# Performance work log

Measured on AMD Instinct MI355X. Metric: run time of the kernel, lower is better.

Reference implementation:

```python
import jax, jax.numpy as jnp
import numpy as np

T, B, E, H = 2048, 4, 1024, 16
HD = E // H
SCALE = HD ** -0.5


def setup_inputs() -> dict:
    key = jax.random.key(0)
    k1, k2, k3 = jax.random.split(key, 3)
    # xavier-ish scaling on weights for numerical sanity
    inputs = jax.random.normal(k1, (T, B, E), dtype=jnp.float32)
    in_proj_weight = jax.random.normal(k2, (3 * E, E), dtype=jnp.float32) * (2.0 / (4 * E)) ** 0.5
    out_proj_weight = jax.random.normal(k3, (E, E), dtype=jnp.float32) * (1.0 / E) ** 0.5
    return {"inputs": inputs, "in_proj_weight": in_proj_weight, "out_proj_weight": out_proj_weight}


def reference(inputs, in_proj_weight, out_proj_weight):
    t, b, e = inputs.shape
    # fused QKV projection: [T,B,E] @ [E,3E] -> [T, B*H, 3, HD]
    qkv = jnp.einsum('tbe,fe->tbf', inputs, in_proj_weight)
    qkv = qkv.reshape(t, b * H, 3, HD)
    q, k, v = qkv[:, :, 0, :], qkv[:, :, 1, :], qkv[:, :, 2, :]  # [T, B*H, HD]
    # scaled attention scores per (batch*head): [B*H, T, T]
    scores = SCALE * jnp.einsum('tnd,snd->nts', q, k)
    probs = jax.nn.softmax(scores, axis=-1)
    # dropout p=0.0 -> identity
    ctx = jnp.einsum('nts,snd->tnd', probs, v).reshape(t, b, e)
    # output projection (applied to attention context, matching intended math / backward)
    return jnp.einsum('tbe,oe->tbo', ctx, out_proj_weight)
```

## Files before the change

kernel.cpp:

```cpp
#include <hip/hip_runtime.h>
#include <stdint.h>
#include <stddef.h>


typedef __attribute__((ext_vector_type(8))) short bf16x8;
typedef __attribute__((ext_vector_type(4))) float f32x4;
typedef __attribute__((ext_vector_type(4))) unsigned int u32x4;

#define MFMA16(a, b, c) __builtin_amdgcn_mfma_f32_16x16x32_bf16((a), (b), (c), 0, 0, 0)

__device__ __forceinline__ unsigned short f2bf(float f) {
  unsigned u = __builtin_bit_cast(unsigned, f);
  u += 0x7fffu + ((u >> 16) & 1u);
  return (unsigned short)(u >> 16);
}

__device__ __forceinline__ float fast_exp2(float x) {
#if __has_builtin(__builtin_amdgcn_exp2f)
  return __builtin_amdgcn_exp2f(x);
#else
  return exp2f(x);
#endif
}

__device__ __forceinline__ unsigned cvtpk(float lo, float hi) {
  unsigned r;
  asm volatile("v_cvt_pk_bf16_f32 %0, %1, %2" : "=v"(r) : "v"(lo), "v"(hi));
  return r;
}

__device__ __forceinline__ void lane_swap32(unsigned &a, unsigned &b) {
#if __has_builtin(__builtin_amdgcn_permlane32_swap)
  auto r = __builtin_amdgcn_permlane32_swap(a, b, false, false);
  a = r[0]; b = r[1];
#else
  const bool hi = (threadIdx.x & 32) != 0;
  unsigned sa = (unsigned)__shfl_xor((int)a, 32, 64);
  unsigned sb = (unsigned)__shfl_xor((int)b, 32, 64);
  unsigned na = hi ? sb : a;
  unsigned nb = hi ? b : sa;
  a = na; b = nb;
#endif
}

__device__ __forceinline__ void lane_swap16(unsigned &a, unsigned &b) {
#if __has_builtin(__builtin_amdgcn_permlane16_swap)
  auto r = __builtin_amdgcn_permlane16_swap(a, b, false, false);
  a = r[0]; b = r[1];
#else
  const bool odd = (threadIdx.x & 16) != 0;
  unsigned sa = (unsigned)__shfl_xor((int)a, 16, 64);
  unsigned sb = (unsigned)__shfl_xor((int)b, 16, 64);
  unsigned na = odd ? sb : a;
  unsigned nb = odd ? b : sa;
  a = na; b = nb;
#endif
}

__device__ __forceinline__ void gload_lds16(const void* g, void* l) {
  __builtin_amdgcn_global_load_lds((const __attribute__((address_space(1))) void*)g,
                                   (__attribute__((address_space(3))) void*)l,
                                   16, 0, 0);
}

__global__ __launch_bounds__(256) void k_cvt3(const float* __restrict__ X,
                                              const float* __restrict__ W1,
                                              const float* __restrict__ Wo,
                                              unsigned short* __restrict__ Xb,
                                              unsigned short* __restrict__ W1b,
                                              unsigned short* __restrict__ Wob) {
  int i = blockIdx.x * 256 + threadIdx.x;
  const float* src;
  unsigned short* dst;
  int j;
  if (i < 2097152) { src = X; dst = Xb; j = i; }
  else if (i < 2097152 + 786432) { src = W1; dst = W1b; j = i - 2097152; }
  else { src = Wo; dst = Wob; j = i - (2097152 + 786432); }
  const float4 v = ((const float4*)src)[j];
  ushort4 o;
  o.x = f2bf(v.x); o.y = f2bf(v.y); o.z = f2bf(v.z); o.w = f2bf(v.w);
  ((ushort4*)dst)[j] = o;
}

__global__ __launch_bounds__(256, 2) void k_gemm_qkv(
    const unsigned short* __restrict__ A,
    const unsigned short* __restrict__ Bt,
    unsigned short* __restrict__ Qb,
    unsigned short* __restrict__ Kb,
    unsigned short* __restrict__ VTb) {
  constexpr int K = 1024;
  __shared__ __align__(16) unsigned short Sm[8704];
  unsigned short* As = Sm;
  unsigned short* Bs = Sm + 4096;

  const int tid = threadIdx.x;
  const int l = tid & 63, w = tid >> 6;
  const int lr = l & 15, lg = l >> 4;
  const int bm = blockIdx.x, bn = blockIdx.y;
  const int wr = (w >> 1) * 64, wc = (w & 1) * 64;

  f32x4 acc[4][4] = {};

  const int o0 = tid * 16, o1 = tid * 16 + 4096;
  const int r0 = o0 >> 6, c0 = o0 & 63;
  const int r1 = o1 >> 6, c1 = o1 & 63;
  const char* gA0 = (const char*)A + (size_t)(bm * 128 + r0) * (K * 2) + c0;
  const char* gA1 = (const char*)A + (size_t)(bm * 128 + r1) * (K * 2) + c1;
  const char* gB0 = (const char*)Bt + (size_t)(bn * 128 + r0) * (K * 2) + c0;
  const char* gB1 = (const char*)Bt + (size_t)(bn * 128 + r1) * (K * 2) + c1;
  char* lA0 = (char*)As + o0;
  char* lA1 = (char*)As + o1;
  char* lB0 = (char*)Bs + o0;
  char* lB1 = (char*)Bs + o1;

  for (int kt = 0; kt < K / 32; ++kt) {
    const int kb = kt * 64;
    gload_lds16(gA0 + kb, lA0);
    gload_lds16(gA1 + kb, lA1);
    gload_lds16(gB0 + kb, lB0);
    gload_lds16(gB1 + kb, lB1);
    __syncthreads();
    bf16x8 af[4], bfr[4];
#pragma unroll
    for (int mf = 0; mf < 4; ++mf)
      af[mf] = *(const bf16x8*)&As[(wr + mf * 16 + lr) * 32 + lg * 8];
#pragma unroll
    for (int nf = 0; nf < 4; ++nf)
      bfr[nf] = *(const bf16x8*)&Bs[(wc + nf * 16 + lr) * 32 + lg * 8];
#pragma unroll
    for (int mf = 0; mf < 4; ++mf)
#pragma unroll
      for (int nf = 0; nf < 4; ++nf)
        acc[mf][nf] = MFMA16(af[mf], bfr[nf], acc[mf][nf]);
    __syncthreads();
  }

  const int f0 = bn * 128 + wc;
  const int s3g = (f0 >> 6) % 3;
  const int hqg = f0 / 192;

  if (s3g != 2) {
    unsigned short* dst = (s3g == 0) ? Qb : Kb;
    const float qscale = (s3g == 0) ? 0.18033688011112042f : 1.0f;
#pragma unroll
    for (int nf = 0; nf < 4; ++nf) {
      const int d = nf * 16 + lr;
#pragma unroll
      for (int mf = 0; mf < 4; ++mf) {
#pragma unroll
        for (int i = 0; i < 4; ++i) {
          const int r = bm * 128 + wr + mf * 16 + lg * 4 + i;
          const int t = r >> 2, bb2 = r & 3;
          dst[((size_t)(bb2 * 16 + hqg) * 2048 + t) * 64 + d] = f2bf(acc[mf][nf][i] * qscale);
        }
      }
    }
  } else {
#pragma unroll
    for (int nf = 0; nf < 4; ++nf) {
      const int d = nf * 16 + lr;
#pragma unroll
      for (int mf = 0; mf < 4; ++mf) {
#pragma unroll
        for (int i = 0; i < 4; ++i) {
          const int rl = wr + mf * 16 + lg * 4 + i;
          Sm[rl * 68 + d] = f2bf(acc[mf][nf][i]);
        }
      }
    }
  }
  __syncthreads();
  if (s3g == 2) {
    const int u = (w >> 1) * 64 + l;
    const int d = u >> 1, th = u & 1;
#pragma unroll
    for (int bb = 0; bb < 4; ++bb) {
      const size_t base = ((size_t)(bb * 16 + hqg) * 64 + d) * 2048 + bm * 32 + th * 16;
#pragma unroll
      for (int tq = 0; tq < 4; ++tq) {
        ushort4 pk;
        pk.x = Sm[((th * 16 + tq * 4 + 0) * 4 + bb) * 68 + d];
        pk.y = Sm[((th * 16 + tq * 4 + 1) * 4 + bb) * 68 + d];
        pk.z = Sm[((th * 16 + tq * 4 + 2) * 4 + bb) * 68 + d];
        pk.w = Sm[((th * 16 + tq * 4 + 3) * 4 + bb) * 68 + d];
        *(ushort4*)&VTb[base + tq * 4] = pk;
      }
    }
  }
}

__global__ __launch_bounds__(256, 2) void k_attn(
    const unsigned short* __restrict__ Qb, const unsigned short* __restrict__ Kb,
    const unsigned short* __restrict__ VTb, unsigned short* __restrict__ Cx) {
  __shared__ __align__(16) unsigned short Ks[2][64 * 64];
  __shared__ __align__(16) unsigned short Vt[2][64 * 64];

  const int tid = threadIdx.x;
  const int l = tid & 63, w = tid >> 6;
  const int lq = l & 15, lg = l >> 4;
  const int n = blockIdx.x, qt = blockIdx.y;

  const unsigned short* Qh = Qb + (size_t)n * (2048 * 64);
  const unsigned short* Kh = Kb + (size_t)n * (2048 * 64);
  const unsigned short* Vh = VTb + (size_t)n * (64 * 2048);

  bf16x8 aq[4][2];
#pragma unroll
  for (int qf = 0; qf < 4; ++qf)
#pragma unroll
    for (int kd = 0; kd < 2; ++kd)
      aq[qf][kd] = *(const bf16x8*)&Qh[(size_t)(qt * 256 + w * 64 + qf * 16 + lq) * 64 +
                                       kd * 32 + lg * 8];

  f32x4 o[4][4] = {};
  float lsum[4] = {0.f, 0.f, 0.f, 0.f};

  char* Ksl = (char*)&Ks[0][0];
  char* Vtl = (char*)&Vt[0][0];

  auto STAGE = [&](int buf, int st) {
    const int s0 = st * 64;
#pragma unroll
    for (int it = 0; it < 2; ++it) {
      const int off = (it * 256 + tid) * 16;
      const int row = off >> 7;
      const int colb = (off & 127) ^ ((row & 7) << 4);
      gload_lds16((const char*)Kh + ((size_t)(s0 + row) << 7) + colb, Ksl + buf * 8192 + off);
      gload_lds16((const char*)Vh + ((size_t)row << 12) + (s0 << 1) + colb, Vtl + buf * 8192 + off);
    }
  };

  STAGE(0, 0);
  asm volatile("s_waitcnt vmcnt(0)" ::: "memory");
  __builtin_amdgcn_s_barrier();

#pragma unroll 2
  for (int st = 0; st < 32; ++st) {
    const int cur = st & 1;
    if (st + 1 < 32) STAGE(cur ^ 1, st + 1);

    const char* Kc = Ksl + cur * 8192;
    const char* Vc = Vtl + cur * 8192;

    __builtin_amdgcn_s_setprio(1);
#pragma unroll
    for (int kb = 0; kb < 2; ++kb) {
      bf16x8 kf[2][2];
#pragma unroll
      for (int sfl = 0; sfl < 2; ++sfl) {
        const int rowk = (2 * kb + sfl) * 16 + lq;
        const int sw = (rowk & 7) << 4;
        kf[sfl][0] = *(const bf16x8*)(Kc + ((rowk * 128 + lg * 16) ^ sw));
        kf[sfl][1] = *(const bf16x8*)(Kc + ((rowk * 128 + 64 + lg * 16) ^ sw));
      }

      bf16x8 pq[4];
#pragma unroll
      for (int qf = 0; qf < 4; ++qf) {
        f32x4 s0 = {0.f, 0.f, 0.f, 0.f};
        f32x4 s1 = {0.f, 0.f, 0.f, 0.f};
        s0 = MFMA16(kf[0][0], aq[qf][0], s0);
        s0 = MFMA16(kf[0][1], aq[qf][1], s0);
        s1 = MFMA16(kf[1][0], aq[qf][0], s1);
        s1 = MFMA16(kf[1][1], aq[qf][1], s1);
        float accs = 0.f;
#pragma unroll
        for (int i = 0; i < 4; ++i) {
          s0[i] = fast_exp2(s0[i]);
          s1[i] = fast_exp2(s1[i]);
          accs += s0[i] + s1[i];
        }
        lsum[qf] += accs;
        unsigned w0 = cvtpk(s0[0], s0[1]);
        unsigned w1 = cvtpk(s0[2], s0[3]);
        unsigned w2 = cvtpk(s1[0], s1[1]);
        unsigned w3 = cvtpk(s1[2], s1[3]);
        lane_swap32(w0, w2);
        lane_swap32(w1, w3);
        lane_swap16(w0, w2);
        lane_swap16(w1, w3);
        u32x4 t4 = {w0, w1, w2, w3};
        pq[qf] = __builtin_bit_cast(bf16x8, t4);
      }

#pragma unroll
      for (int df = 0; df < 4; ++df) {
        const int rowd = df * 16 + lq;
        const int sw = (rowd & 7) << 4;
        bf16x8 vf = *(const bf16x8*)(Vc + ((rowd * 128 + kb * 64 + lg * 16) ^ sw));
#pragma unroll
        for (int qf = 0; qf < 4; ++qf)
          o[df][qf] = MFMA16(vf, pq[qf], o[df][qf]);
      }
    }
    __builtin_amdgcn_s_setprio(0);

    asm volatile("s_waitcnt vmcnt(0)" ::: "memory");
    __builtin_amdgcn_s_barrier();
  }

  const int bb = n >> 4, h = n & 15;
#pragma unroll
  for (int qf = 0; qf < 4; ++qf) {
    float li = lsum[qf];
    li += __shfl_xor(li, 16, 64);
    li += __shfl_xor(li, 32, 64);
    const float inv = 1.0f / li;
    const int q = qt * 256 + w * 64 + qf * 16 + lq;
#pragma unroll
    for (int df = 0; df < 4; ++df) {
      ushort4 pk;
      pk.x = f2bf(o[df][qf][0] * inv);
      pk.y = f2bf(o[df][qf][1] * inv);
      pk.z = f2bf(o[df][qf][2] * inv);
      pk.w = f2bf(o[df][qf][3] * inv);
      *(ushort4*)&Cx[(size_t)(q * 4 + bb) * 1024 + h * 64 + df * 16 + lg * 4] = pk;
    }
  }
}

__global__ __launch_bounds__(256, 2) void k_gemm_out(
    const unsigned short* __restrict__ A,
    const unsigned short* __restrict__ Bt,
    float* __restrict__ C) {
  constexpr int K = 1024;
  __shared__ __align__(16) unsigned short As[128 * 32];
  __shared__ __align__(16) unsigned short Bs[128 * 32];
  const int tid = threadIdx.x;
  const int l = tid & 63, w = tid >> 6;
  const int lr = l & 15, lg = l >> 4;
  const int bm = blockIdx.x, bn = blockIdx.y;
  const int wr = (w >> 1) * 64, wc = (w & 1) * 64;

  f32x4 acc[4][4] = {};

  const int o0 = tid * 16, o1 = tid * 16 + 4096;
  const int r0 = o0 >> 6, c0 = o0 & 63;
  const int r1 = o1 >> 6, c1 = o1 & 63;
  const char* gA0 = (const char*)A + (size_t)(bm * 128 + r0) * (K * 2) + c0;
  const char* gA1 = (const char*)A + (size_t)(bm * 128 + r1) * (K * 2) + c1;
  const char* gB0 = (const char*)Bt + (size_t)(bn * 128 + r0) * (K * 2) + c0;
  const char* gB1 = (const char*)Bt + (size_t)(bn * 128 + r1) * (K * 2) + c1;
  char* lA0 = (char*)As + o0;
  char* lA1 = (char*)As + o1;
  char* lB0 = (char*)Bs + o0;
  char* lB1 = (char*)Bs + o1;

  for (int kt = 0; kt < K / 32; ++kt) {
    const int kb = kt * 64;
    gload_lds16(gA0 + kb, lA0);
    gload_lds16(gA1 + kb, lA1);
    gload_lds16(gB0 + kb, lB0);
    gload_lds16(gB1 + kb, lB1);
    __syncthreads();
    bf16x8 af[4], bfr[4];
#pragma unroll
    for (int mf = 0; mf < 4; ++mf)
      af[mf] = *(const bf16x8*)&As[(wr + mf * 16 + lr) * 32 + lg * 8];
#pragma unroll
    for (int nf = 0; nf < 4; ++nf)
      bfr[nf] = *(const bf16x8*)&Bs[(wc + nf * 16 + lr) * 32 + lg * 8];
#pragma unroll
    for (int mf = 0; mf < 4; ++mf)
#pragma unroll
      for (int nf = 0; nf < 4; ++nf)
        acc[mf][nf] = MFMA16(af[mf], bfr[nf], acc[mf][nf]);
    __syncthreads();
  }

#pragma unroll
  for (int mf = 0; mf < 4; ++mf)
#pragma unroll
    for (int i = 0; i < 4; ++i) {
      const int r = bm * 128 + wr + mf * 16 + lg * 4 + i;
#pragma unroll
      for (int nf = 0; nf < 4; ++nf)
        C[(size_t)r * 1024 + bn * 128 + wc + nf * 16 + lr] = acc[mf][nf][i];
    }
}

extern "C" void kernel_launch(void* const* d_in, const int* in_sizes, int n_in,
                              void* d_out, int out_size, void* d_ws, size_t ws_size,
                              hipStream_t stream) {
  const float* X = (const float*)d_in[0];
  const float* W1 = (const float*)d_in[1];
  const float* Wo = (const float*)d_in[2];
  float* out = (float*)d_out;

  char* ws = (char*)d_ws;
  unsigned short* Xb  = (unsigned short*)(ws);
  unsigned short* W1b = (unsigned short*)(ws + 16777216);
  unsigned short* Wob = (unsigned short*)(ws + 23068672);
  unsigned short* Qb  = (unsigned short*)(ws + 25165824);
  unsigned short* Kb  = (unsigned short*)(ws + 41943040);
  unsigned short* VTb = (unsigned short*)(ws + 58720256);
  unsigned short* Cx  = (unsigned short*)(ws + 75497472);

  k_cvt3<<<12288, 256, 0, stream>>>(X, W1, Wo, Xb, W1b, Wob);
  k_gemm_qkv<<<dim3(64, 24), 256, 0, stream>>>(Xb, W1b, Qb, Kb, VTb);
  k_attn<<<dim3(64, 8), 256, 0, stream>>>(Qb, Kb, VTb, Cx);
  k_gemm_out<<<dim3(64, 8), 256, 0, stream>>>(Cx, Wob, out);
}
```

Before: 186.7 us.

## Rewrite projection GEMMs with 128x256 tiles, double-buffered swizzled LDS and prefetch

Both the QKV and output projection GEMMs now use 512-thread blocks computing 128x256 tiles over a K step of 64. Global-to-LDS loads for the next step are issued while the current step runs its MFMAs, using a double buffer, vmcnt waits, raw barriers and setprio. The LDS layout is XOR-swizzled to avoid bank conflicts. This cuts barrier count and exposed load latency per FLOP, but uses 96KB of LDS per block, which may limit occupancy, and halves the number of blocks.

```diff
diff --git a/kernel.cpp b/kernel.cpp
--- a/kernel.cpp
+++ b/kernel.cpp
@@ -82,60 +82,85 @@
   ((ushort4*)dst)[j] = o;
 }
 
-__global__ __launch_bounds__(256, 2) void k_gemm_qkv(
+
+__global__ __launch_bounds__(512, 2) void k_gemm_qkv(
     const unsigned short* __restrict__ A,
     const unsigned short* __restrict__ Bt,
     unsigned short* __restrict__ Qb,
     unsigned short* __restrict__ Kb,
     unsigned short* __restrict__ VTb) {
-  constexpr int K = 1024;
-  __shared__ __align__(16) unsigned short Sm[8704];
-  unsigned short* As = Sm;
-  unsigned short* Bs = Sm + 4096;
+  __shared__ __align__(16) char Sm[98304];
+  char* lAs = Sm;
+  char* lBs = Sm + 32768;
 
   const int tid = threadIdx.x;
-  const int l = tid & 63, w = tid >> 6;
+  const int l = tid & 63;
+  const int wid = tid >> 6;
   const int lr = l & 15, lg = l >> 4;
+  const int wr = wid >> 2, wc = wid & 3;
   const int bm = blockIdx.x, bn = blockIdx.y;
-  const int wr = (w >> 1) * 64, wc = (w & 1) * 64;
 
   f32x4 acc[4][4] = {};
-
-  const int o0 = tid * 16, o1 = tid * 16 + 4096;
-  const int r0 = o0 >> 6, c0 = o0 & 63;
-  const int r1 = o1 >> 6, c1 = o1 & 63;
-  const char* gA0 = (const char*)A + (size_t)(bm * 128 + r0) * (K * 2) + c0;
-  const char* gA1 = (const char*)A + (size_t)(bm * 128 + r1) * (K * 2) + c1;
-  const char* gB0 = (const char*)Bt + (size_t)(bn * 128 + r0) * (K * 2) + c0;
-  const char* gB1 = (const char*)Bt + (size_t)(bn * 128 + r1) * (K * 2) + c1;
-  char* lA0 = (char*)As + o0;
-  char* lA1 = (char*)As + o1;
-  char* lB0 = (char*)Bs + o0;
-  char* lB1 = (char*)Bs + o1;
-
-  for (int kt = 0; kt < K / 32; ++kt) {
-    const int kb = kt * 64;
-    gload_lds16(gA0 + kb, lA0);
-    gload_lds16(gA1 + kb, lA1);
-    gload_lds16(gB0 + kb, lB0);
-    gload_lds16(gB1 + kb, lB1);
-    __syncthreads();
-    bf16x8 af[4], bfr[4];
-#pragma unroll
-    for (int mf = 0; mf < 4; ++mf)
-      af[mf] = *(const bf16x8*)&As[(wr + mf * 16 + lr) * 32 + lg * 8];
-#pragma unroll
-    for (int nf = 0; nf < 4; ++nf)
-      bfr[nf] = *(const bf16x8*)&Bs[(wc + nf * 16 + lr) * 32 + lg * 8];
-#pragma unroll
-    for (int mf = 0; mf < 4; ++mf)
+  const int colF = (lg * 16) ^ (((lr >> 1) & 3) << 4);
+
+  auto STAGE_A = [&](int buf, int kt2, int uk) {
+    const int row = tid >> 2;
+    const int colb = (tid & 3) * 16;
+    const int sw = ((row >> 1) & 3) << 4;
+    gload_lds16((const char*)A + (size_t)(bm * 128 + row) * 2048 + kt2 * 128 + uk * 64 +
+                    (colb ^ sw),
+                lAs + (buf * 2 + uk) * 8192 + tid * 16);
+  };
+  auto STAGE_B = [&](int buf, int kt2, int uk) {
+#pragma unroll
+    for (int i = 0; i < 2; ++i) {
+      const int idx = i * 512 + tid;
+      const int row = idx >> 2;
+      const int colb = (idx & 3) * 16;
+      const int sw = ((row >> 1) & 3) << 4;
+      gload_lds16((const char*)Bt + (size_t)(bn * 256 + row) * 2048 + kt2 * 128 + uk * 64 +
+                      (colb ^ sw),
+                  lBs + (buf * 2 + uk) * 16384 + idx * 16);
+    }
+  };
+
+  STAGE_A(0, 0, 0); STAGE_B(0, 0, 0);
+  STAGE_A(0, 0, 1); STAGE_B(0, 0, 1);
+  asm volatile("s_waitcnt vmcnt(3)" ::: "memory");
+  __builtin_amdgcn_s_barrier();
+
+#pragma unroll 2
+  for (int kt = 0; kt < 16; ++kt) {
+    const int buf = kt & 1, nbuf = buf ^ 1;
+    const int ktn = (kt + 1 < 16) ? kt + 1 : 15;
+
+#pragma unroll
+    for (int uk = 0; uk < 2; ++uk) {
+      bf16x8 a[4], b[4];
+#pragma unroll
+      for (int mf = 0; mf < 4; ++mf)
+        a[mf] = *(const bf16x8*)(lAs + (buf * 2 + uk) * 8192 + (wr * 64 + mf * 16 + lr) * 64 + colF);
 #pragma unroll
       for (int nf = 0; nf < 4; ++nf)
-        acc[mf][nf] = MFMA16(af[mf], bfr[nf], acc[mf][nf]);
-    __syncthreads();
-  }
-
-  const int f0 = bn * 128 + wc;
+        b[nf] = *(const bf16x8*)(lBs + (buf * 2 + uk) * 16384 + (wc * 64 + nf * 16 + lr) * 64 + colF);
+      STAGE_A(nbuf, ktn, uk);
+      STAGE_B(nbuf, ktn, uk);
+      __builtin_amdgcn_s_setprio(1);
+#pragma unroll
+      for (int mf = 0; mf < 4; ++mf)
+#pragma unroll
+        for (int nf = 0; nf < 4; ++nf)
+          acc[mf][nf] = MFMA16(a[mf], b[nf], acc[mf][nf]);
+      __builtin_amdgcn_s_setprio(0);
+      asm volatile("s_waitcnt vmcnt(3)" ::: "memory");
+      __builtin_amdgcn_s_barrier();
+    }
+  }
+
+  asm volatile("s_waitcnt vmcnt(0)" ::: "memory");
+  __syncthreads();
+
+  const int f0 = bn * 256 + wc * 64;
   const int s3g = (f0 >> 6) % 3;
   const int hqg = f0 / 192;
 
@@ -149,13 +174,14 @@
       for (int mf = 0; mf < 4; ++mf) {
 #pragma unroll
         for (int i = 0; i < 4; ++i) {
-          const int r = bm * 128 + wr + mf * 16 + lg * 4 + i;
+          const int r = bm * 128 + wr * 64 + mf * 16 + lg * 4 + i;
           const int t = r >> 2, bb2 = r & 3;
           dst[((size_t)(bb2 * 16 + hqg) * 2048 + t) * 64 + d] = f2bf(acc[mf][nf][i] * qscale);
         }
       }
     }
   } else {
+    unsigned short* Tb = (unsigned short*)(Sm + wc * 24576);
 #pragma unroll
     for (int nf = 0; nf < 4; ++nf) {
       const int d = nf * 16 + lr;
@@ -163,15 +189,16 @@
       for (int mf = 0; mf < 4; ++mf) {
 #pragma unroll
         for (int i = 0; i < 4; ++i) {
-          const int rl = wr + mf * 16 + lg * 4 + i;
-          Sm[rl * 68 + d] = f2bf(acc[mf][nf][i]);
+          const int rl = wr * 64 + mf * 16 + lg * 4 + i;
+          Tb[rl * 68 + d] = f2bf(acc[mf][nf][i]);
         }
       }
     }
   }
   __syncthreads();
   if (s3g == 2) {
-    const int u = (w >> 1) * 64 + l;
+    unsigned short* Tb = (unsigned short*)(Sm + wc * 24576);
+    const int u = wr * 64 + l;
     const int d = u >> 1, th = u & 1;
 #pragma unroll
     for (int bb = 0; bb < 4; ++bb) {
@@ -179,14 +206,99 @@
 #pragma unroll
       for (int tq = 0; tq < 4; ++tq) {
         ushort4 pk;
-        pk.x = Sm[((th * 16 + tq * 4 + 0) * 4 + bb) * 68 + d];
-        pk.y = Sm[((th * 16 + tq * 4 + 1) * 4 + bb) * 68 + d];
-        pk.z = Sm[((th * 16 + tq * 4 + 2) * 4 + bb) * 68 + d];
-        pk.w = Sm[((th * 16 + tq * 4 + 3) * 4 + bb) * 68 + d];
+        pk.x = Tb[((th * 16 + tq * 4 + 0) * 4 + bb) * 68 + d];
+        pk.y = Tb[((th * 16 + tq * 4 + 1) * 4 + bb) * 68 + d];
+        pk.z = Tb[((th * 16 + tq * 4 + 2) * 4 + bb) * 68 + d];
+        pk.w = Tb[((th * 16 + tq * 4 + 3) * 4 + bb) * 68 + d];
         *(ushort4*)&VTb[base + tq * 4] = pk;
       }
     }
   }
+}
+
+__global__ __launch_bounds__(512, 2) void k_gemm_out(
+    const unsigned short* __restrict__ A,
+    const unsigned short* __restrict__ Bt,
+    float* __restrict__ C) {
+  __shared__ __align__(16) char Sm[98304];
+  char* lAs = Sm;
+  char* lBs = Sm + 32768;
+
+  const int tid = threadIdx.x;
+  const int l = tid & 63;
+  const int wid = tid >> 6;
+  const int lr = l & 15, lg = l >> 4;
+  const int wr = wid >> 2, wc = wid & 3;
+  const int bm = blockIdx.x, bn = blockIdx.y;
+
+  f32x4 acc[4][4] = {};
+  const int colF = (lg * 16) ^ (((lr >> 1) & 3) << 4);
+
+  auto STAGE_A = [&](int buf, int kt2, int uk) {
+    const int row = tid >> 2;
+    const int colb = (tid & 3) * 16;
+    const int sw = ((row >> 1) & 3) << 4;
+    gload_lds16((const char*)A + (size_t)(bm * 128 + row) * 2048 + kt2 * 128 + uk * 64 +
+                    (colb ^ sw),
+                lAs + (buf * 2 + uk) * 8192 + tid * 16);
+  };
+  auto STAGE_B = [&](int buf, int kt2, int uk) {
+#pragma unroll
+    for (int i = 0; i < 2; ++i) {
+      const int idx = i * 512 + tid;
+      const int row = idx >> 2;
+      const int colb = (idx & 3) * 16;
+      const int sw = ((row >> 1) & 3) << 4;
+      gload_lds16((const char*)Bt + (size_t)(bn * 256 + row) * 2048 + kt2 * 128 + uk * 64 +
+                      (colb ^ sw),
+                  lBs + (buf * 2 + uk) * 16384 + idx * 16);
+    }
+  };
+
+  STAGE_A(0, 0, 0); STAGE_B(0, 0, 0);
+  STAGE_A(0, 0, 1); STAGE_B(0, 0, 1);
+  asm volatile("s_waitcnt vmcnt(3)" ::: "memory");
+  __builtin_amdgcn_s_barrier();
+
+#pragma unroll 2
+  for (int kt = 0; kt < 16; ++kt) {
+    const int buf = kt & 1, nbuf = buf ^ 1;
+    const int ktn = (kt + 1 < 16) ? kt + 1 : 15;
+
+#pragma unroll
+    for (int uk = 0; uk < 2; ++uk) {
+      bf16x8 a[4], b[4];
+#pragma unroll
+      for (int mf = 0; mf < 4; ++mf)
+        a[mf] = *(const bf16x8*)(lAs + (buf * 2 + uk) * 8192 + (wr * 64 + mf * 16 + lr) * 64 + colF);
+#pragma unroll
+      for (int nf = 0; nf < 4; ++nf)
+        b[nf] = *(const bf16x8*)(lBs + (buf * 2 + uk) * 16384 + (wc * 64 + nf * 16 + lr) * 64 + colF);
+      STAGE_A(nbuf, ktn, uk);
+      STAGE_B(nbuf, ktn, uk);
+      __builtin_amdgcn_s_setprio(1);
+#pragma unroll
+      for (int mf = 0; mf < 4; ++mf)
+#pragma unroll
+        for (int nf = 0; nf < 4; ++nf)
+          acc[mf][nf] = MFMA16(a[mf], b[nf], acc[mf][nf]);
+      __builtin_amdgcn_s_setprio(0);
+      asm volatile("s_waitcnt vmcnt(3)" ::: "memory");
+      __builtin_amdgcn_s_barrier();
+    }
+  }
+
+  asm volatile("s_waitcnt vmcnt(0)" ::: "memory");
+
+#pragma unroll
+  for (int mf = 0; mf < 4; ++mf)
+#pragma unroll
+    for (int i = 0; i < 4; ++i) {
+      const int r = bm * 128 + wr * 64 + mf * 16 + lg * 4 + i;
+#pragma unroll
+      for (int nf = 0; nf < 4; ++nf)
+        C[(size_t)r * 1024 + bn * 256 + wc * 64 + nf * 16 + lr] = acc[mf][nf][i];
+    }
 }
 
 __global__ __launch_bounds__(256, 2) void k_attn(
@@ -319,66 +431,6 @@
   }
 }
 
-__global__ __launch_bounds__(256, 2) void k_gemm_out(
-    const unsigned short* __restrict__ A,
-    const unsigned short* __restrict__ Bt,
-    float* __restrict__ C) {
-  constexpr int K = 1024;
-  __shared__ __align__(16) unsigned short As[128 * 32];
-  __shared__ __align__(16) unsigned short Bs[128 * 32];
-  const int tid = threadIdx.x;
-  const int l = tid & 63, w = tid >> 6;
-  const int lr = l & 15, lg = l >> 4;
-  const int bm = blockIdx.x, bn = blockIdx.y;
-  const int wr = (w >> 1) * 64, wc = (w & 1) * 64;
-
-  f32x4 acc[4][4] = {};
-
-  const int o0 = tid * 16, o1 = tid * 16 + 4096;
-  const int r0 = o0 >> 6, c0 = o0 & 63;
-  const int r1 = o1 >> 6, c1 = o1 & 63;
-  const char* gA0 = (const char*)A + (size_t)(bm * 128 + r0) * (K * 2) + c0;
-  const char* gA1 = (const char*)A + (size_t)(bm * 128 + r1) * (K * 2) + c1;
-  const char* gB0 = (const char*)Bt + (size_t)(bn * 128 + r0) * (K * 2) + c0;
-  const char* gB1 = (const char*)Bt + (size_t)(bn * 128 + r1) * (K * 2) + c1;
-  char* lA0 = (char*)As + o0;
-  char* lA1 = (char*)As + o1;
-  char* lB0 = (char*)Bs + o0;
-  char* lB1 = (char*)Bs + o1;
-
-  for (int kt = 0; kt < K / 32; ++kt) {
-    const int kb = kt * 64;
-    gload_lds16(gA0 + kb, lA0);
-    gload_lds16(gA1 + kb, lA1);
-    gload_lds16(gB0 + kb, lB0);
-    gload_lds16(gB1 + kb, lB1);
-    __syncthreads();
-    bf16x8 af[4], bfr[4];
-#pragma unroll
-    for (int mf = 0; mf < 4; ++mf)
-      af[mf] = *(const bf16x8*)&As[(wr + mf * 16 + lr) * 32 + lg * 8];
-#pragma unroll
-    for (int nf = 0; nf < 4; ++nf)
-      bfr[nf] = *(const bf16x8*)&Bs[(wc + nf * 16 + lr) * 32 + lg * 8];
-#pragma unroll
-    for (int mf = 0; mf < 4; ++mf)
-#pragma unroll
-      for (int nf = 0; nf < 4; ++nf)
-        acc[mf][nf] = MFMA16(af[mf], bfr[nf], acc[mf][nf]);
-    __syncthreads();
-  }
-
-#pragma unroll
-  for (int mf = 0; mf < 4; ++mf)
-#pragma unroll
-    for (int i = 0; i < 4; ++i) {
-      const int r = bm * 128 + wr + mf * 16 + lg * 4 + i;
-#pragma unroll
-      for (int nf = 0; nf < 4; ++nf)
-        C[(size_t)r * 1024 + bn * 128 + wc + nf * 16 + lr] = acc[mf][nf][i];
-    }
-}
-
 extern "C" void kernel_launch(void* const* d_in, const int* in_sizes, int n_in,
                               void* d_out, int out_size, void* d_ws, size_t ws_size,
                               hipStream_t stream) {
@@ -397,7 +449,7 @@
   unsigned short* Cx  = (unsigned short*)(ws + 75497472);
 
   k_cvt3<<<12288, 256, 0, stream>>>(X, W1, Wo, Xb, W1b, Wob);
-  k_gemm_qkv<<<dim3(64, 24), 256, 0, stream>>>(Xb, W1b, Qb, Kb, VTb);
+  k_gemm_qkv<<<dim3(64, 12), 512, 0, stream>>>(Xb, W1b, Qb, Kb, VTb);
   k_attn<<<dim3(64, 8), 256, 0, stream>>>(Qb, Kb, VTb, Cx);
-  k_gemm_out<<<dim3(64, 8), 256, 0, stream>>>(Cx, Wob, out);
-}
+  k_gemm_out<<<dim3(64, 4), 512, 0, stream>>>(Cx, Wob, out);
+}
```

Result: faster. 178.6 us (-4.4%).
